# Kernel optimization log

Hardware: AMD Instinct MI355X
Metric: run time of the kernel (lower is better)

## Reference

```python
import jax, jax.numpy as jnp
import numpy as np

FT = 0.2  # clip floor (init arg ft)

def _norm_mat(m):
    # matrix / (count of nonzeros along last dim + 1e-30)
    deg = jnp.sum(m != 0, axis=-1, keepdims=True).astype(m.dtype)
    return m / (deg + 1e-30)

def _l2n(x):
    return x / (jnp.linalg.norm(x, axis=-1, keepdims=True) + 1e-30)

def setup_inputs():
    B, L, D, H, O = 2, 2048, 64, 64, 128
    N = 2 * L
    ks = jax.random.split(jax.random.key(0), 30)
    u = lambda i, s: jax.random.uniform(ks[i], s, jnp.float32)
    g = lambda i, s: jax.random.normal(ks[i], s, jnp.float32) * 0.05
    inp = {}
    inp['word_outputs_0'] = g(0, (B, L, D))
    inp['word_outputs_1'] = g(1, (B, L, D))
    inp['node_hidden'] = g(2, (B, D))
    inp['op_embedding'] = g(3, (B, O, D))
    inp['word_exist_sequence'] = (u(4, (B, N)) < 0.8).astype(jnp.float32)
    inp['word_exist_matrix'] = (u(5, (B, N, N)) < 0.8).astype(jnp.float32)
    inp['word_operator'] = (u(6, (B, N, O)) < 0.02).astype(jnp.float32)
    inp['word_word'] = (u(7, (B, N, N)) < 0.01).astype(jnp.float32)
    inp['depend_0'] = (u(8, (B, L, L)) < 0.05).astype(jnp.float32)
    inp['depend_1'] = (u(9, (B, L, L)) < 0.05).astype(jnp.float32)
    inp['goal_word'] = u(10, (B, N))
    names = [('Wg', (D, H)), ('bg', (H,)), ('Wwk', (D, H)), ('bwk', (H,)),
             ('Wws', (D, H)), ('bws', (H,)), ('Wo', (D, D)), ('bo', (D,)),
             ('Wupd', (3 * H, D)), ('bupd', (D,)), ('Wf', (3 * H + D, D)), ('bf', (D,)),
             ('Wf2', (2 * D, D)), ('bf2', (D,)), ('Wout', (D, D)), ('bout', (D,))]
    for i, (nm, s) in enumerate(names):
        inp[nm] = g(11 + i, s)
    return inp

def _forward(w0, w1, nh, opE, wes, wem, wop, ww, d0, d1, gw,
             Wg, bg, Wwk, bwk, Wws, bws, Wo, bo, Wupd, bupd, Wf, bf, Wf2, bf2, Wout, bout):
    all_w = jnp.concatenate([w0, w1], axis=1)                      # [B,N,D]
    goal_trans = (nh @ Wg + bg)[:, None, :]                        # [B,1,H] (broadcast = expand)
    word_g = _l2n(goal_trans * gw[..., None])                      # [B,N,H]
    word_w_k = _l2n(jnp.matmul(_norm_mat(ww * wem), all_w @ Wwk + bwk))
    ws0 = jnp.matmul(_norm_mat(d0), w0 @ Wws + bws)
    ws1 = jnp.matmul(_norm_mat(d1), w1 @ Wws + bws)
    word_w_s = _l2n(jnp.concatenate([ws0, ws1], axis=1))           # [B,N,H]
    neigh = jnp.concatenate([word_g, word_w_k, word_w_s], axis=-1)  # [B,N,3H]
    forget = jax.nn.sigmoid(jnp.concatenate([all_w, word_g, word_w_k, word_w_s], axis=-1) @ Wf + bf)
    word_updated = jnp.maximum(forget, FT) * all_w + (1.0 - forget) * jax.nn.relu(neigh @ Wupd + bupd)
    adj_op = _norm_mat(jnp.swapaxes(wes[..., None] * wop, 1, 2))   # [B,O,N]
    word_op = jnp.matmul(adj_op, word_updated @ Wo + bo)           # [B,O,D]
    forget2 = jax.nn.sigmoid(jnp.concatenate([opE, word_op], axis=-1) @ Wf2 + bf2)
    op_out = jnp.maximum(forget2, FT) * opE + (1.0 - forget2) * jax.nn.relu(word_op @ Wout + bout)
    # original returns (split(word_updated), op_embedding); concat along node axis here
    return jnp.concatenate([word_updated, op_out], axis=1)         # [B,N+O,D]

def reference(word_outputs_0, word_outputs_1, node_hidden, op_embedding,
              word_exist_sequence, word_exist_matrix, word_operator, word_word,
              depend_0, depend_1, goal_word,
              Wg, bg, Wwk, bwk, Wws, bws, Wo, bo, Wupd, bupd, Wf, bf, Wf2, bf2, Wout, bout):
    return _forward(word_outputs_0, word_outputs_1, node_hidden, op_embedding,
                    word_exist_sequence, word_exist_matrix, word_operator, word_word,
                    depend_0, depend_1, goal_word,
                    Wg, bg, Wwk, bwk, Wws, bws, Wo, bo, Wupd, bupd, Wf, bf, Wf2, bf2, Wout, bout)
```

## Files before the change

kernel.cpp:

```cpp
#include <hip/hip_runtime.h>
#include <cstdint>

typedef unsigned short u16;
typedef unsigned long long u64;

__device__ __forceinline__ u16 f2b(float f){
  union { float f; uint32_t i; } v; v.f = f;
  uint32_t r = v.i + 0x7FFFu + ((v.i >> 16) & 1u);
  return (u16)(r >> 16);
}
__device__ __forceinline__ float b2f(u16 u){
  union { uint32_t i; float f; } v; v.i = ((uint32_t)u) << 16; return v.f;
}
__device__ __forceinline__ float sigmoidf(float x){ return 1.0f / (1.0f + __expf(-x)); }

__device__ __forceinline__ void gl_lds4(const void* g, void* l){
  __builtin_amdgcn_global_load_lds((const __attribute__((address_space(1))) void*)g,
                                   (__attribute__((address_space(3))) void*)l, 4, 0, 0);
}

__device__ __forceinline__ void mask_ptrs(int t,
    const float* ww, const float* wem, const float* d0, const float* d1,
    const float4** ap, const float4** bp, bool* two){
  if (t < 32768){
    int row = t >> 2, chunk = t & 3;
    *ap = (const float4*)(ww  + (size_t)row*4096 + chunk*1024);
    *bp = (const float4*)(wem + (size_t)row*4096 + chunk*1024);
    *two = true;
  } else {
    int idx = t - 32768, rowp = idx >> 1, chunk = idx & 1;
    const float* base;
    if (rowp < 4096) base = d0 + (size_t)rowp*2048 + chunk*1024;
    else { int rr = rowp - 4096; base = d1 + (size_t)rr*2048 + chunk*1024; }
    *ap = (const float4*)base; *bp = (const float4*)base; *two = false;
  }
}

__global__ __launch_bounds__(256) void k_mask(
    const float* __restrict__ ww, const float* __restrict__ wem,
    const float* __restrict__ d0, const float* __restrict__ d1,
    const float* __restrict__ wes, const float* __restrict__ wop,
    const float* __restrict__ w0, const float* __restrict__ w1,
    const float* __restrict__ nh, const float* __restrict__ Wg, const float* __restrict__ bg,
    const float* __restrict__ Wf, const float* __restrict__ Wupd, const float* __restrict__ Wo,
    u16* __restrict__ psumB, int* __restrict__ pcntB,
    u16* __restrict__ psumD, int* __restrict__ pcntD,
    u64* __restrict__ bitOp, float* __restrict__ ghat,
    uint32_t* __restrict__ pkWf, uint32_t* __restrict__ pkWu, uint32_t* __restrict__ pkWo){
  __shared__ int q[4][272];
  __shared__ float rows[4][8][64];
  int tid = threadIdx.x, wave = tid >> 6, lane = tid & 63;
  int bid = blockIdx.x;
  if (bid >= 2048){
    if (bid >= 2304){
      int aux = bid - 2304;
      if (aux == 16){
        if (tid < 128){
          int b = tid >> 6, h = tid & 63;
          float g = bg[h];
          for (int d = 0; d < 64; ++d) g += nh[b*64 + d] * Wg[d*64 + h];
          float ss = g * g;
          #pragma unroll
          for (int o = 32; o > 0; o >>= 1) ss += __shfl_xor(ss, o, 64);
          ghat[b*64 + h] = g / (sqrtf(ss) + 1e-30f);
        }
        return;
      }
      for (int k = tid; k < 1024; k += 256){
        int i = aux*1024 + k;
        const float* src; uint32_t* dst; int li;
        if (i < 8192){ src = Wf; dst = pkWf; li = i; }
        else if (i < 14336){ src = Wupd; dst = pkWu; li = i - 8192; }
        else { src = Wo; dst = pkWo; li = i - 14336; }
        int k2 = li >> 6, ln = li & 63;
        dst[li] = (uint32_t)f2b(src[(2*k2)*64 + ln]) | ((uint32_t)f2b(src[(2*k2+1)*64 + ln]) << 16);
      }
      return;
    }
    int w = (bid - 2048)*4 + wave;
    int ng0 = w * 8;
    #pragma unroll
    for (int i = 0; i < 8; ++i){
      int n = ng0 + i;
      float vx = wop[(size_t)n*128 + lane];
      float vy = wop[(size_t)n*128 + 64 + lane];
      float e  = wes[n];
      u64 m0 = __ballot((e != 0.f) && (vx != 0.f));
      u64 m1 = __ballot((e != 0.f) && (vy != 0.f));
      if (lane == 0) bitOp[(size_t)n*2]     = m0;
      if (lane == 1) bitOp[(size_t)n*2 + 1] = m1;
    }
    return;
  }
  int wid = bid*4 + wave;
  const float4 *ap, *bp; bool two;
  mask_ptrs(wid, ww, wem, d0, d1, &ap, &bp, &two);
  float4 a0 = ap[lane], a1 = ap[64 + lane], a2 = ap[128 + lane], a3 = ap[192 + lane];
  float4 b0 = {0,0,0,0}, b1 = {0,0,0,0}, b2 = {0,0,0,0}, b3 = {0,0,0,0};
  if (two){ b0 = bp[lane]; b1 = bp[64 + lane]; b2 = bp[128 + lane]; b3 = bp[192 + lane]; }

  for (int it = 0; it < 6; ++it){
    int t = wid + it*8192;
    const float *srcA, *srcB;
    int jbase, thresh;
    u16* ps; int* pc;
    if (t < 32768){
      int row = t >> 2, chunk = t & 3;
      int b = row >> 12;
      srcA = w0 + (size_t)b*131072 + lane;
      srcB = w1 + (size_t)b*131072 - 131072 + lane;
      jbase = chunk*1024; thresh = 2048;
      ps = psumB + (size_t)t*64; pc = pcntB + t;
    } else {
      int idx = t - 32768, rowp = idx >> 1, chunk = idx & 1;
      if (rowp < 4096){
        int b = rowp >> 11;
        srcA = w0 + (size_t)b*131072 + lane;
      } else {
        int rr = rowp - 4096, b = rr >> 11;
        srcA = w1 + (size_t)b*131072 + lane;
      }
      srcB = srcA;
      jbase = chunk*1024; thresh = 4096;
      ps = psumD + (size_t)idx*64; pc = pcntD + idx;
    }
    float4 an0 = {0,0,0,0}, an1 = {0,0,0,0}, an2 = {0,0,0,0}, an3 = {0,0,0,0};
    float4 bn0 = {0,0,0,0}, bn1 = {0,0,0,0}, bn2 = {0,0,0,0}, bn3 = {0,0,0,0};
    bool twon = false;
    if (it < 5){
      const float4 *apn, *bpn;
      mask_ptrs(t + 8192, ww, wem, d0, d1, &apn, &bpn, &twon);
      an0 = apn[lane]; an1 = apn[64 + lane]; an2 = apn[128 + lane]; an3 = apn[192 + lane];
      if (twon){ bn0 = bpn[lane]; bn1 = bpn[64 + lane]; bn2 = bpn[128 + lane]; bn3 = bpn[192 + lane]; }
    }
    u64 myw = 0;
#define B4(i, va, vb) { \
  u64 m0 = __ballot((va.x != 0.f) && (!two || (vb.x != 0.f))); \
  u64 m1 = __ballot((va.y != 0.f) && (!two || (vb.y != 0.f))); \
  u64 m2 = __ballot((va.z != 0.f) && (!two || (vb.z != 0.f))); \
  u64 m3 = __ballot((va.w != 0.f) && (!two || (vb.w != 0.f))); \
  if (lane == (i)*4 + 0) myw = m0; \
  if (lane == (i)*4 + 1) myw = m1; \
  if (lane == (i)*4 + 2) myw = m2; \
  if (lane == (i)*4 + 3) myw = m3; }
    B4(0, a0, b0) B4(1, a1, b1) B4(2, a2, b2) B4(3, a3, b3)
#undef B4
    int c = __popcll(myw);
    int pre = c;
    #pragma unroll
    for (int off = 1; off < 64; off <<= 1){
      int tt = __shfl_up(pre, off, 64);
      if (lane >= off) pre += tt;
    }
    int total = __shfl(pre, 63, 64);
    int base = pre - c;
    int colhi = (lane >> 2) * 256 + (lane & 3);
    u64 m = myw;
    while (m){
      int p = __builtin_ctzll(m); m &= m - 1;
      q[wave][base++] = colhi + p*4;
    }
    int totP = (total + 7) & ~7;
    if (lane < totP - total) q[wave][total + lane] = 0;
    float acc = 0.f;
#define GPJ(qv) (((jbase + (qv)) < thresh ? srcA : srcB) + (size_t)(jbase + (qv))*64)
    for (int b8 = 0; b8 < totP; b8 += 8){
      int4 c0 = *(const int4*)&q[wave][b8];
      int4 c1 = *(const int4*)&q[wave][b8 + 4];
      gl_lds4(GPJ(c0.x), &rows[wave][0][0]);
      gl_lds4(GPJ(c0.y), &rows[wave][1][0]);
      gl_lds4(GPJ(c0.z), &rows[wave][2][0]);
      gl_lds4(GPJ(c0.w), &rows[wave][3][0]);
      gl_lds4(GPJ(c1.x), &rows[wave][4][0]);
      gl_lds4(GPJ(c1.y), &rows[wave][5][0]);
      gl_lds4(GPJ(c1.z), &rows[wave][6][0]);
      gl_lds4(GPJ(c1.w), &rows[wave][7][0]);
      asm volatile("s_waitcnt vmcnt(0)" ::: "memory");
      #pragma unroll
      for (int r = 0; r < 8; ++r){
        float v = rows[wave][r][lane];
        acc += (b8 + r < total) ? v : 0.f;
      }
    }
#undef GPJ
    ps[lane] = f2b(acc);
    if (lane == 0) pc[0] = total;
    if (it < 5){
      a0 = an0; a1 = an1; a2 = an2; a3 = an3;
      if (twon){ b0 = bn0; b1 = bn1; b2 = bn2; b3 = bn3; }
      two = twon;
    }
  }
}

__global__ __launch_bounds__(256) void k_fin(
    const u16* __restrict__ psumB, const int* __restrict__ pcntB,
    const u16* __restrict__ psumD, const int* __restrict__ pcntD,
    const float* __restrict__ Wwk, const float* __restrict__ bwk,
    const float* __restrict__ Wws, const float* __restrict__ bws,
    u16* __restrict__ wwkn, u16* __restrict__ wwsn){
  __shared__ float sWk[4096], sWs[4096];
  int tid = threadIdx.x, lane = tid & 63, wave = tid >> 6;
  for (int i = tid; i < 1024; i += 256){
    ((float4*)sWk)[i] = ((const float4*)Wwk)[i];
    ((float4*)sWs)[i] = ((const float4*)Wws)[i];
  }
  __syncthreads();
  for (int r = 0; r < 4; ++r){
    int wid = blockIdx.x*4 + wave + r*4096;
    float S; float y; const float* sW; u16* outp; size_t oidx;
    if (wid < 8192){
      S = b2f(psumB[((size_t)wid*4 + 0)*64 + lane]) + b2f(psumB[((size_t)wid*4 + 1)*64 + lane])
        + b2f(psumB[((size_t)wid*4 + 2)*64 + lane]) + b2f(psumB[((size_t)wid*4 + 3)*64 + lane]);
      int T = pcntB[wid*4] + pcntB[wid*4 + 1] + pcntB[wid*4 + 2] + pcntB[wid*4 + 3];
      y = (float)T * bwk[lane]; sW = sWk; outp = wwkn; oidx = wid;
    } else {
      int rp = wid - 8192;
      S = b2f(psumD[((size_t)rp*2 + 0)*64 + lane]) + b2f(psumD[((size_t)rp*2 + 1)*64 + lane]);
      int T = pcntD[rp*2] + pcntD[rp*2 + 1];
      y = (float)T * bws[lane]; sW = sWs; outp = wwsn;
      int b, n;
      if (rp < 4096){ b = rp >> 11; n = rp & 2047; }
      else { int rr = rp - 4096; b = rr >> 11; n = 2048 + (rr & 2047); }
      oidx = (size_t)b*4096 + n;
    }
    #pragma unroll 8
    for (int d = 0; d < 64; ++d) y += __shfl(S, d, 64) * sW[d*64 + lane];
    float ss = y * y;
    #pragma unroll
    for (int o = 32; o > 0; o >>= 1) ss += __shfl_xor(ss, o, 64);
    outp[oidx*64 + lane] = f2b(y / (sqrtf(ss) + 1e-30f));
  }
}

__global__ __launch_bounds__(256, 2) void k_update(
    const float* __restrict__ w0, const float* __restrict__ w1,
    const float* __restrict__ gw, const float* __restrict__ ghat,
    const u16* __restrict__ wwkn, const u16* __restrict__ wwsn,
    const uint32_t* __restrict__ pkWf, const uint32_t* __restrict__ pkWu,
    const uint32_t* __restrict__ pkWo,
    const float* __restrict__ bf, const float* __restrict__ bupd, const float* __restrict__ bo,
    float* __restrict__ out, float* __restrict__ WUo){
  __shared__ uint32_t pWf[8192];
  __shared__ uint32_t pWu[6144];
  __shared__ uint32_t pWo[2048];
  __shared__ float xsh[4][256];
  int tid = threadIdx.x;
  for (int i = tid; i < 2048; i += 256) ((uint4*)pWf)[i] = ((const uint4*)pkWf)[i];
  for (int i = tid; i < 1536; i += 256) ((uint4*)pWu)[i] = ((const uint4*)pkWu)[i];
  for (int i = tid; i < 512;  i += 256) ((uint4*)pWo)[i] = ((const uint4*)pkWo)[i];
  __syncthreads();
  int lane = tid & 63, wave = tid >> 6;
  float bff = bf[lane], bup = bupd[lane], boo = bo[lane];
  float aw[4], wgv[4], wk[4], wsv[4];
  #pragma unroll
  for (int t = 0; t < 4; ++t){
    int row = blockIdx.x*4 + wave + t*2048;
    int b = row >> 12, n = row & 4095;
    aw[t] = (n < 2048) ? w0[((size_t)(b*2048 + n))*64 + lane]
                       : w1[((size_t)(b*2048 + n - 2048))*64 + lane];
    float gvv = gw[b*4096 + n];
    wgv[t] = (gvv != 0.f) ? ghat[b*64 + lane] : 0.f;
    wk[t]  = b2f(wwkn[(size_t)row*64 + lane]);
    wsv[t] = b2f(wwsn[(size_t)row*64 + lane]);
  }
  #pragma unroll
  for (int t = 0; t < 4; ++t){
    int row = blockIdx.x*4 + wave + t*2048;
    int b = row >> 12, n = row & 4095;
    xsh[wave][lane] = aw[t]; xsh[wave][64 + lane] = wgv[t];
    xsh[wave][128 + lane] = wk[t]; xsh[wave][192 + lane] = wsv[t];
    float f = bff, u = bup;
    #pragma unroll 8
    for (int k2 = 0; k2 < 32; ++k2){
      float2 xv = *(const float2*)&xsh[wave][2*k2];
      uint32_t wf = pWf[k2*64 + lane];
      f += xv.x * b2f((u16)wf) + xv.y * b2f((u16)(wf >> 16));
    }
    #pragma unroll 8
    for (int k2 = 32; k2 < 128; ++k2){
      float2 xv = *(const float2*)&xsh[wave][2*k2];
      uint32_t wf = pWf[k2*64 + lane];
      uint32_t wu = pWu[(k2 - 32)*64 + lane];
      f += xv.x * b2f((u16)wf) + xv.y * b2f((u16)(wf >> 16));
      u += xv.x * b2f((u16)wu) + xv.y * b2f((u16)(wu >> 16));
    }
    f = sigmoidf(f);
    u = fmaxf(u, 0.f);
    float wu = fmaxf(f, 0.2f) * aw[t] + (1.f - f) * u;
    out[((size_t)b*4224 + n)*64 + lane] = wu;
    float o = boo;
    #pragma unroll 8
    for (int k2 = 0; k2 < 32; ++k2){
      uint32_t wo2 = pWo[k2*64 + lane];
      o += __shfl(wu, 2*k2, 64) * b2f((u16)wo2) + __shfl(wu, 2*k2 + 1, 64) * b2f((u16)(wo2 >> 16));
    }
    WUo[(size_t)row*64 + lane] = o;
  }
}

__global__ __launch_bounds__(256) void k_opfin(
    const u64* __restrict__ bitOp, const float* __restrict__ WUo,
    const float* __restrict__ opE,
    const float* __restrict__ Wf2, const float* __restrict__ bf2,
    const float* __restrict__ Wout, const float* __restrict__ bout,
    float* __restrict__ out){
  __shared__ float sW2[8192];
  __shared__ float sWo[4096];
  __shared__ int q[4][96];
  __shared__ float sacc[4][64];
  __shared__ int scnt[4];
  __shared__ float xsh[128];
  int tid = threadIdx.x, lane = tid & 63, wave = tid >> 6;
  for (int i = tid; i < 2048; i += 256) ((float4*)sW2)[i] = ((const float4*)Wf2)[i];
  for (int i = tid; i < 1024; i += 256) ((float4*)sWo)[i] = ((const float4*)Wout)[i];
  int rowIdx = blockIdx.x;
  int b = rowIdx >> 7, o = rowIdx & 127;
  int wrd = o >> 6, bit = o & 63;
  const u64* bp = bitOp + (size_t)b*8192 + (size_t)wave*2048 + wrd;
  u64 lt = (1ULL << lane) - 1ULL;
  u64 vv[16];
  #pragma unroll
  for (int it = 0; it < 16; ++it) vv[it] = bp[(size_t)(it*64 + lane)*2];
  int cnt = 0;
  #pragma unroll
  for (int it = 0; it < 16; ++it){
    bool nz = (vv[it] >> bit) & 1ULL;
    u64 m = __ballot(nz);
    if (nz) q[wave][cnt + (int)__popcll(m & lt)] = wave*1024 + it*64 + lane;
    cnt += (int)__popcll(m);
  }
  const float* Xb = WUo + (size_t)b*4096*64 + lane;
  float acc = 0.f;
  int i = 0;
  for (; i + 8 <= cnt; i += 8){
    int4 c0 = *(const int4*)&q[wave][i];
    int4 c1 = *(const int4*)&q[wave][i + 4];
    float v0 = Xb[(size_t)c0.x*64], v1 = Xb[(size_t)c0.y*64];
    float v2 = Xb[(size_t)c0.z*64], v3 = Xb[(size_t)c0.w*64];
    float v4 = Xb[(size_t)c1.x*64], v5 = Xb[(size_t)c1.y*64];
    float v6 = Xb[(size_t)c1.z*64], v7 = Xb[(size_t)c1.w*64];
    acc += ((v0 + v1) + (v2 + v3)) + ((v4 + v5) + (v6 + v7));
  }
  for (; i < cnt; ++i) acc += Xb[(size_t)q[wave][i]*64];
  sacc[wave][lane] = acc;
  if (lane == 0) scnt[wave] = cnt;
  __syncthreads();
  if (wave == 0){
    float t = sacc[0][lane] + sacc[1][lane] + sacc[2][lane] + sacc[3][lane];
    float deg = (float)(scnt[0] + scnt[1] + scnt[2] + scnt[3]);
    float wo = t / (deg + 1e-30f);
    float e  = opE[(size_t)rowIdx*64 + lane];
    xsh[lane] = e; xsh[64 + lane] = wo;
    float f = bf2[lane], u = bout[lane];
    #pragma unroll 8
    for (int k = 0; k < 128; ++k) f += xsh[k] * sW2[k*64 + lane];
    #pragma unroll 8
    for (int d = 0; d < 64; ++d)  u += xsh[64 + d] * sWo[d*64 + lane];
    f = sigmoidf(f);
    u = fmaxf(u, 0.f);
    float res = fmaxf(f, 0.2f) * e + (1.f - f) * u;
    out[((size_t)b*4224 + 4096 + o)*64 + lane] = res;
  }
}

extern "C" void kernel_launch(void* const* d_in, const int* in_sizes, int n_in,
                              void* d_out, int out_size, void* d_ws, size_t ws_size,
                              hipStream_t stream){
  const float* w0   = (const float*)d_in[0];
  const float* w1   = (const float*)d_in[1];
  const float* nh   = (const float*)d_in[2];
  const float* opE  = (const float*)d_in[3];
  const float* wes  = (const float*)d_in[4];
  const float* wem  = (const float*)d_in[5];
  const float* wop  = (const float*)d_in[6];
  const float* ww   = (const float*)d_in[7];
  const float* d0   = (const float*)d_in[8];
  const float* d1   = (const float*)d_in[9];
  const float* gw   = (const float*)d_in[10];
  const float* Wg   = (const float*)d_in[11];
  const float* bg   = (const float*)d_in[12];
  const float* Wwk  = (const float*)d_in[13];
  const float* bwk  = (const float*)d_in[14];
  const float* Wws  = (const float*)d_in[15];
  const float* bws  = (const float*)d_in[16];
  const float* Wo   = (const float*)d_in[17];
  const float* bo   = (const float*)d_in[18];
  const float* Wupd = (const float*)d_in[19];
  const float* bupd = (const float*)d_in[20];
  const float* Wf   = (const float*)d_in[21];
  const float* bf   = (const float*)d_in[22];
  const float* Wf2  = (const float*)d_in[23];
  const float* bf2  = (const float*)d_in[24];
  const float* Wout = (const float*)d_in[25];
  const float* bout = (const float*)d_in[26];

  float* ws    = (float*)d_ws;
  float* ghat  = ws;
  uint32_t* pkWf = (uint32_t*)(ws + 128);
  uint32_t* pkWu = (uint32_t*)(ws + 8320);
  uint32_t* pkWo = (uint32_t*)(ws + 14464);
  u64*  bitOp  = (u64*)(ws + 16512);
  u16*  psumB  = (u16*)(ws + 49280);
  int*  pcntB  = (int*)(ws + 1097856);
  u16*  psumD  = (u16*)(ws + 1130624);
  int*  pcntD  = (int*)(ws + 1654912);
  u16*  wwkn   = (u16*)(ws + 1671296);
  u16*  wwsn   = (u16*)(ws + 1933440);
  float* WUo   = ws + 2195584;
  float* out   = (float*)d_out;

  k_mask<<<2321, 256, 0, stream>>>(ww, wem, d0, d1, wes, wop, w0, w1,
                                   nh, Wg, bg, Wf, Wupd, Wo,
                                   psumB, pcntB, psumD, pcntD,
                                   bitOp, ghat, pkWf, pkWu, pkWo);
  k_fin<<<1024, 256, 0, stream>>>(psumB, pcntB, psumD, pcntD,
                                  Wwk, bwk, Wws, bws, wwkn, wwsn);
  k_update<<<512, 256, 0, stream>>>(w0, w1, gw, ghat, wwkn, wwsn,
                                    pkWf, pkWu, pkWo, bf, bupd, bo, out, WUo);
  k_opfin<<<256, 256, 0, stream>>>(bitOp, WUo, opE, Wf2, bf2, Wout, bout, out);
}
```

Before: 448.9 us.

## Fuse neighbor-finalize into update kernel and register-pipeline sparse row gathers

The separate k_fin kernel is merged into the update kernel, so the normalized word-key and word-structure vectors stay in registers instead of making a bf16 round trip through global memory, and one launch is dropped. In the masking kernel, the LDS-staged global_load_lds gathers with a full vmcnt wait per 8 rows are replaced by direct per-lane register loads in 16-row batches, double-buffered so the next batch is issued before the current one is accumulated. Prefetch of the next mask tile now happens after the index list is built rather than before, which changes register pressure and overlap. The fused kernel reuses one LDS buffer for both weight sets, at the cost of an extra barrier and serialized weight loads per block.

```diff
diff --git a/kernel.cpp b/kernel.cpp
--- a/kernel.cpp
+++ b/kernel.cpp
@@ -14,29 +14,7 @@
 }
 __device__ __forceinline__ float sigmoidf(float x){ return 1.0f / (1.0f + __expf(-x)); }
 
-__device__ __forceinline__ void gl_lds4(const void* g, void* l){
-  __builtin_amdgcn_global_load_lds((const __attribute__((address_space(1))) void*)g,
-                                   (__attribute__((address_space(3))) void*)l, 4, 0, 0);
-}
-
-__device__ __forceinline__ void mask_ptrs(int t,
-    const float* ww, const float* wem, const float* d0, const float* d1,
-    const float4** ap, const float4** bp, bool* two){
-  if (t < 32768){
-    int row = t >> 2, chunk = t & 3;
-    *ap = (const float4*)(ww  + (size_t)row*4096 + chunk*1024);
-    *bp = (const float4*)(wem + (size_t)row*4096 + chunk*1024);
-    *two = true;
-  } else {
-    int idx = t - 32768, rowp = idx >> 1, chunk = idx & 1;
-    const float* base;
-    if (rowp < 4096) base = d0 + (size_t)rowp*2048 + chunk*1024;
-    else { int rr = rowp - 4096; base = d1 + (size_t)rr*2048 + chunk*1024; }
-    *ap = (const float4*)base; *bp = (const float4*)base; *two = false;
-  }
-}
-
-__global__ __launch_bounds__(256) void k_mask(
+__global__ __launch_bounds__(256) void k_bits(
     const float* __restrict__ ww, const float* __restrict__ wem,
     const float* __restrict__ d0, const float* __restrict__ d1,
     const float* __restrict__ wes, const float* __restrict__ wop,
@@ -47,8 +25,7 @@
     u16* __restrict__ psumD, int* __restrict__ pcntD,
     u64* __restrict__ bitOp, float* __restrict__ ghat,
     uint32_t* __restrict__ pkWf, uint32_t* __restrict__ pkWu, uint32_t* __restrict__ pkWo){
-  __shared__ int q[4][272];
-  __shared__ float rows[4][8][64];
+  __shared__ int q[4][288];
   int tid = threadIdx.x, wave = tid >> 6, lane = tid & 63;
   int bid = blockIdx.x;
   if (bid >= 2048){
@@ -92,58 +69,58 @@
     }
     return;
   }
-  int wid = bid*4 + wave;
-  const float4 *ap, *bp; bool two;
-  mask_ptrs(wid, ww, wem, d0, d1, &ap, &bp, &two);
-  float4 a0 = ap[lane], a1 = ap[64 + lane], a2 = ap[128 + lane], a3 = ap[192 + lane];
-  float4 b0 = {0,0,0,0}, b1 = {0,0,0,0}, b2 = {0,0,0,0}, b3 = {0,0,0,0};
-  if (two){ b0 = bp[lane]; b1 = bp[64 + lane]; b2 = bp[128 + lane]; b3 = bp[192 + lane]; }
-
+  int wid = __builtin_amdgcn_readfirstlane(bid*4 + wave);
+  float4 a0, a1, a2, a3, b0v, b1v, b2v, b3v;
+#define ISSUE_MASKS(tt) { \
+  int t_ = (tt); \
+  if (t_ < 32768){ \
+    int row_ = t_ >> 2, ch_ = t_ & 3; \
+    const float4* ra_ = (const float4*)(ww  + (size_t)row_*4096 + ch_*1024) + lane; \
+    const float4* rb_ = (const float4*)(wem + (size_t)row_*4096 + ch_*1024) + lane; \
+    a0 = ra_[0]; a1 = ra_[64]; a2 = ra_[128]; a3 = ra_[192]; \
+    b0v = rb_[0]; b1v = rb_[64]; b2v = rb_[128]; b3v = rb_[192]; \
+  } else { \
+    int idx_ = t_ - 32768, rowp_ = idx_ >> 1, ch_ = idx_ & 1; \
+    const float* A_; \
+    if (rowp_ < 4096) A_ = d0 + (size_t)rowp_*2048 + ch_*1024; \
+    else { int rr_ = rowp_ - 4096; A_ = d1 + (size_t)rr_*2048 + ch_*1024; } \
+    const float4* ra_ = (const float4*)A_ + lane; \
+    a0 = ra_[0]; a1 = ra_[64]; a2 = ra_[128]; a3 = ra_[192]; \
+  } }
+  ISSUE_MASKS(wid)
+  #pragma unroll 1
   for (int it = 0; it < 6; ++it){
     int t = wid + it*8192;
-    const float *srcA, *srcB;
+    bool big = (t < 32768);
+    const float *sA, *sB;
     int jbase, thresh;
     u16* ps; int* pc;
-    if (t < 32768){
+    if (big){
       int row = t >> 2, chunk = t & 3;
       int b = row >> 12;
-      srcA = w0 + (size_t)b*131072 + lane;
-      srcB = w1 + (size_t)b*131072 - 131072 + lane;
+      sA = w0 + (size_t)b*131072;
+      sB = w1 + (size_t)b*131072 - 131072;
       jbase = chunk*1024; thresh = 2048;
       ps = psumB + (size_t)t*64; pc = pcntB + t;
     } else {
       int idx = t - 32768, rowp = idx >> 1, chunk = idx & 1;
-      if (rowp < 4096){
-        int b = rowp >> 11;
-        srcA = w0 + (size_t)b*131072 + lane;
-      } else {
-        int rr = rowp - 4096, b = rr >> 11;
-        srcA = w1 + (size_t)b*131072 + lane;
-      }
-      srcB = srcA;
+      if (rowp < 4096){ int b = rowp >> 11; sA = w0 + (size_t)b*131072; }
+      else { int rr = rowp - 4096, b = rr >> 11; sA = w1 + (size_t)b*131072; }
+      sB = sA;
       jbase = chunk*1024; thresh = 4096;
       ps = psumD + (size_t)idx*64; pc = pcntD + idx;
     }
-    float4 an0 = {0,0,0,0}, an1 = {0,0,0,0}, an2 = {0,0,0,0}, an3 = {0,0,0,0};
-    float4 bn0 = {0,0,0,0}, bn1 = {0,0,0,0}, bn2 = {0,0,0,0}, bn3 = {0,0,0,0};
-    bool twon = false;
-    if (it < 5){
-      const float4 *apn, *bpn;
-      mask_ptrs(t + 8192, ww, wem, d0, d1, &apn, &bpn, &twon);
-      an0 = apn[lane]; an1 = apn[64 + lane]; an2 = apn[128 + lane]; an3 = apn[192 + lane];
-      if (twon){ bn0 = bpn[lane]; bn1 = bpn[64 + lane]; bn2 = bpn[128 + lane]; bn3 = bpn[192 + lane]; }
-    }
     u64 myw = 0;
 #define B4(i, va, vb) { \
-  u64 m0 = __ballot((va.x != 0.f) && (!two || (vb.x != 0.f))); \
-  u64 m1 = __ballot((va.y != 0.f) && (!two || (vb.y != 0.f))); \
-  u64 m2 = __ballot((va.z != 0.f) && (!two || (vb.z != 0.f))); \
-  u64 m3 = __ballot((va.w != 0.f) && (!two || (vb.w != 0.f))); \
+  u64 m0 = __ballot((va.x != 0.f) && (!big || (vb.x != 0.f))); \
+  u64 m1 = __ballot((va.y != 0.f) && (!big || (vb.y != 0.f))); \
+  u64 m2 = __ballot((va.z != 0.f) && (!big || (vb.z != 0.f))); \
+  u64 m3 = __ballot((va.w != 0.f) && (!big || (vb.w != 0.f))); \
   if (lane == (i)*4 + 0) myw = m0; \
   if (lane == (i)*4 + 1) myw = m1; \
   if (lane == (i)*4 + 2) myw = m2; \
   if (lane == (i)*4 + 3) myw = m3; }
-    B4(0, a0, b0) B4(1, a1, b1) B4(2, a2, b2) B4(3, a3, b3)
+    B4(0, a0, b0v) B4(1, a1, b1v) B4(2, a2, b2v) B4(3, a3, b3v)
 #undef B4
     int c = __popcll(myw);
     int pre = c;
@@ -160,110 +137,97 @@
       int p = __builtin_ctzll(m); m &= m - 1;
       q[wave][base++] = colhi + p*4;
     }
-    int totP = (total + 7) & ~7;
+    int totP = (total + 15) & ~15;
     if (lane < totP - total) q[wave][total + lane] = 0;
+    if (it < 5) ISSUE_MASKS(t + 8192)
     float acc = 0.f;
-#define GPJ(qv) (((jbase + (qv)) < thresh ? srcA : srcB) + (size_t)(jbase + (qv))*64)
-    for (int b8 = 0; b8 < totP; b8 += 8){
-      int4 c0 = *(const int4*)&q[wave][b8];
-      int4 c1 = *(const int4*)&q[wave][b8 + 4];
-      gl_lds4(GPJ(c0.x), &rows[wave][0][0]);
-      gl_lds4(GPJ(c0.y), &rows[wave][1][0]);
-      gl_lds4(GPJ(c0.z), &rows[wave][2][0]);
-      gl_lds4(GPJ(c0.w), &rows[wave][3][0]);
-      gl_lds4(GPJ(c1.x), &rows[wave][4][0]);
-      gl_lds4(GPJ(c1.y), &rows[wave][5][0]);
-      gl_lds4(GPJ(c1.z), &rows[wave][6][0]);
-      gl_lds4(GPJ(c1.w), &rows[wave][7][0]);
-      asm volatile("s_waitcnt vmcnt(0)" ::: "memory");
-      #pragma unroll
-      for (int r = 0; r < 8; ++r){
-        float v = rows[wave][r][lane];
-        acc += (b8 + r < total) ? v : 0.f;
+    int nb = totP >> 4;
+    float g0[16], g1[16];
+#define GISS(arr, bi) { int bse = (bi) << 4; \
+  _Pragma("unroll") for (int k2 = 0; k2 < 16; ++k2){ \
+    int j = __builtin_amdgcn_readfirstlane(jbase + q[wave][bse + k2]); \
+    const float* pp = ((j < thresh) ? sA : sB) + (size_t)j*64; \
+    arr[k2] = pp[lane]; } }
+#define GACC(arr, bi) { int bse = (bi) << 4; \
+  _Pragma("unroll") for (int k2 = 0; k2 < 16; ++k2) \
+    acc += (bse + k2 < total) ? arr[k2] : 0.f; }
+    if (nb > 0) GISS(g0, 0)
+    for (int bi = 0; bi < nb; bi += 2){
+      if (bi + 1 < nb) GISS(g1, bi + 1)
+      GACC(g0, bi)
+      if (bi + 1 < nb){
+        if (bi + 2 < nb) GISS(g0, bi + 2)
+        GACC(g1, bi + 1)
       }
     }
-#undef GPJ
+#undef GISS
+#undef GACC
     ps[lane] = f2b(acc);
     if (lane == 0) pc[0] = total;
-    if (it < 5){
-      a0 = an0; a1 = an1; a2 = an2; a3 = an3;
-      if (twon){ b0 = bn0; b1 = bn1; b2 = bn2; b3 = bn3; }
-      two = twon;
-    }
-  }
-}
-
-__global__ __launch_bounds__(256) void k_fin(
+  }
+#undef ISSUE_MASKS
+}
+
+__global__ __launch_bounds__(256, 2) void k_mid(
     const u16* __restrict__ psumB, const int* __restrict__ pcntB,
     const u16* __restrict__ psumD, const int* __restrict__ pcntD,
     const float* __restrict__ Wwk, const float* __restrict__ bwk,
     const float* __restrict__ Wws, const float* __restrict__ bws,
-    u16* __restrict__ wwkn, u16* __restrict__ wwsn){
-  __shared__ float sWk[4096], sWs[4096];
-  int tid = threadIdx.x, lane = tid & 63, wave = tid >> 6;
-  for (int i = tid; i < 1024; i += 256){
-    ((float4*)sWk)[i] = ((const float4*)Wwk)[i];
-    ((float4*)sWs)[i] = ((const float4*)Wws)[i];
-  }
-  __syncthreads();
-  for (int r = 0; r < 4; ++r){
-    int wid = blockIdx.x*4 + wave + r*4096;
-    float S; float y; const float* sW; u16* outp; size_t oidx;
-    if (wid < 8192){
-      S = b2f(psumB[((size_t)wid*4 + 0)*64 + lane]) + b2f(psumB[((size_t)wid*4 + 1)*64 + lane])
-        + b2f(psumB[((size_t)wid*4 + 2)*64 + lane]) + b2f(psumB[((size_t)wid*4 + 3)*64 + lane]);
-      int T = pcntB[wid*4] + pcntB[wid*4 + 1] + pcntB[wid*4 + 2] + pcntB[wid*4 + 3];
-      y = (float)T * bwk[lane]; sW = sWk; outp = wwkn; oidx = wid;
-    } else {
-      int rp = wid - 8192;
-      S = b2f(psumD[((size_t)rp*2 + 0)*64 + lane]) + b2f(psumD[((size_t)rp*2 + 1)*64 + lane]);
-      int T = pcntD[rp*2] + pcntD[rp*2 + 1];
-      y = (float)T * bws[lane]; sW = sWs; outp = wwsn;
-      int b, n;
-      if (rp < 4096){ b = rp >> 11; n = rp & 2047; }
-      else { int rr = rp - 4096; b = rr >> 11; n = 2048 + (rr & 2047); }
-      oidx = (size_t)b*4096 + n;
-    }
-    #pragma unroll 8
-    for (int d = 0; d < 64; ++d) y += __shfl(S, d, 64) * sW[d*64 + lane];
-    float ss = y * y;
-    #pragma unroll
-    for (int o = 32; o > 0; o >>= 1) ss += __shfl_xor(ss, o, 64);
-    outp[oidx*64 + lane] = f2b(y / (sqrtf(ss) + 1e-30f));
-  }
-}
-
-__global__ __launch_bounds__(256, 2) void k_update(
     const float* __restrict__ w0, const float* __restrict__ w1,
     const float* __restrict__ gw, const float* __restrict__ ghat,
-    const u16* __restrict__ wwkn, const u16* __restrict__ wwsn,
     const uint32_t* __restrict__ pkWf, const uint32_t* __restrict__ pkWu,
     const uint32_t* __restrict__ pkWo,
     const float* __restrict__ bf, const float* __restrict__ bupd, const float* __restrict__ bo,
     float* __restrict__ out, float* __restrict__ WUo){
-  __shared__ uint32_t pWf[8192];
-  __shared__ uint32_t pWu[6144];
-  __shared__ uint32_t pWo[2048];
+  __shared__ uint32_t ldsU[16384];
   __shared__ float xsh[4][256];
-  int tid = threadIdx.x;
+  int tid = threadIdx.x, lane = tid & 63, wave = tid >> 6;
+  float* sWk = (float*)ldsU;
+  float* sWs = (float*)ldsU + 4096;
+  for (int i = tid; i < 1024; i += 256){
+    ((float4*)sWk)[i] = ((const float4*)Wwk)[i];
+    ((float4*)sWs)[i] = ((const float4*)Wws)[i];
+  }
+  __syncthreads();
+  float bwkL = bwk[lane], bwsL = bws[lane];
+  float wk[4], wsv[4], aw[4], wgv[4];
+  #pragma unroll
+  for (int t = 0; t < 4; ++t){
+    int row = blockIdx.x*4 + wave + t*2048;
+    int b = row >> 12, n = row & 4095;
+    float S = b2f(psumB[((size_t)row*4 + 0)*64 + lane]) + b2f(psumB[((size_t)row*4 + 1)*64 + lane])
+            + b2f(psumB[((size_t)row*4 + 2)*64 + lane]) + b2f(psumB[((size_t)row*4 + 3)*64 + lane]);
+    int T = pcntB[row*4] + pcntB[row*4 + 1] + pcntB[row*4 + 2] + pcntB[row*4 + 3];
+    float y = (float)T * bwkL;
+    #pragma unroll 8
+    for (int d = 0; d < 64; ++d) y += __shfl(S, d, 64) * sWk[d*64 + lane];
+    float ss = y * y;
+    #pragma unroll
+    for (int o = 32; o > 0; o >>= 1) ss += __shfl_xor(ss, o, 64);
+    wk[t] = y / (sqrtf(ss) + 1e-30f);
+    int rp = (n < 2048) ? (b*2048 + n) : (4096 + b*2048 + (n - 2048));
+    float S2 = b2f(psumD[((size_t)rp*2 + 0)*64 + lane]) + b2f(psumD[((size_t)rp*2 + 1)*64 + lane]);
+    int T2 = pcntD[rp*2] + pcntD[rp*2 + 1];
+    float y2 = (float)T2 * bwsL;
+    #pragma unroll 8
+    for (int d = 0; d < 64; ++d) y2 += __shfl(S2, d, 64) * sWs[d*64 + lane];
+    float ss2 = y2 * y2;
+    #pragma unroll
+    for (int o = 32; o > 0; o >>= 1) ss2 += __shfl_xor(ss2, o, 64);
+    wsv[t] = y2 / (sqrtf(ss2) + 1e-30f);
+    aw[t] = (n < 2048) ? w0[((size_t)(b*2048 + n))*64 + lane]
+                       : w1[((size_t)(b*2048 + n - 2048))*64 + lane];
+    wgv[t] = (gw[b*4096 + n] != 0.f) ? ghat[b*64 + lane] : 0.f;
+  }
+  __syncthreads();
+  uint32_t* pWf = ldsU;
+  uint32_t* pWu = ldsU + 8192;
+  uint32_t* pWo = ldsU + 14336;
   for (int i = tid; i < 2048; i += 256) ((uint4*)pWf)[i] = ((const uint4*)pkWf)[i];
   for (int i = tid; i < 1536; i += 256) ((uint4*)pWu)[i] = ((const uint4*)pkWu)[i];
   for (int i = tid; i < 512;  i += 256) ((uint4*)pWo)[i] = ((const uint4*)pkWo)[i];
   __syncthreads();
-  int lane = tid & 63, wave = tid >> 6;
   float bff = bf[lane], bup = bupd[lane], boo = bo[lane];
-  float aw[4], wgv[4], wk[4], wsv[4];
-  #pragma unroll
-  for (int t = 0; t < 4; ++t){
-    int row = blockIdx.x*4 + wave + t*2048;
-    int b = row >> 12, n = row & 4095;
-    aw[t] = (n < 2048) ? w0[((size_t)(b*2048 + n))*64 + lane]
-                       : w1[((size_t)(b*2048 + n - 2048))*64 + lane];
-    float gvv = gw[b*4096 + n];
-    wgv[t] = (gvv != 0.f) ? ghat[b*64 + lane] : 0.f;
-    wk[t]  = b2f(wwkn[(size_t)row*64 + lane]);
-    wsv[t] = b2f(wwsn[(size_t)row*64 + lane]);
-  }
   #pragma unroll
   for (int t = 0; t < 4; ++t){
     int row = blockIdx.x*4 + wave + t*2048;
@@ -405,18 +369,15 @@
   int*  pcntB  = (int*)(ws + 1097856);
   u16*  psumD  = (u16*)(ws + 1130624);
   int*  pcntD  = (int*)(ws + 1654912);
-  u16*  wwkn   = (u16*)(ws + 1671296);
-  u16*  wwsn   = (u16*)(ws + 1933440);
   float* WUo   = ws + 2195584;
   float* out   = (float*)d_out;
 
-  k_mask<<<2321, 256, 0, stream>>>(ww, wem, d0, d1, wes, wop, w0, w1,
+  k_bits<<<2321, 256, 0, stream>>>(ww, wem, d0, d1, wes, wop, w0, w1,
                                    nh, Wg, bg, Wf, Wupd, Wo,
                                    psumB, pcntB, psumD, pcntD,
                                    bitOp, ghat, pkWf, pkWu, pkWo);
-  k_fin<<<1024, 256, 0, stream>>>(psumB, pcntB, psumD, pcntD,
-                                  Wwk, bwk, Wws, bws, wwkn, wwsn);
-  k_update<<<512, 256, 0, stream>>>(w0, w1, gw, ghat, wwkn, wwsn,
-                                    pkWf, pkWu, pkWo, bf, bupd, bo, out, WUo);
+  k_mid<<<512, 256, 0, stream>>>(psumB, pcntB, psumD, pcntD,
+                                 Wwk, bwk, Wws, bws, w0, w1, gw, ghat,
+                                 pkWf, pkWu, pkWo, bf, bupd, bo, out, WUo);
   k_opfin<<<256, 256, 0, stream>>>(bitOp, WUo, opE, Wf2, bf2, Wout, bout, out);
 }
```

Measured after the change: 437.7 us. 1.03x faster.
